# Optimization experiments

Hardware: AMD Instinct MI355X
Metric: run time of the kernel (lower is better)

## Reference

```python
import jax, jax.numpy as jnp
import numpy as np

LEAK = 0.1
K = 16  # nsample

def leaky(x):
    return jnp.where(x > 0, x, LEAK * x)

def setup_inputs() -> dict:
    key = jax.random.key(0)
    ks = jax.random.split(key, 16)
    B, N, C, D = 2, 8192, 128, 128
    s = 0.05
    return {
        "xyz1": jax.random.normal(ks[0], (B, 3, N), jnp.float32),
        "xyz2": jax.random.normal(ks[1], (B, 3, N), jnp.float32),
        "points1": jax.random.normal(ks[2], (B, C, N), jnp.float32),
        "points2": jax.random.normal(ks[3], (B, C, N), jnp.float32),
        "W_t11": jax.random.normal(ks[4], (D, C), jnp.float32) * s,
        "b_t11": jax.random.normal(ks[5], (D,), jnp.float32) * s,
        "W_t22": jax.random.normal(ks[6], (D, C), jnp.float32) * s,
        "b_t22": jax.random.normal(ks[7], (D,), jnp.float32) * s,
        "W_pos": jax.random.normal(ks[8], (D, 3), jnp.float32) * s,
        "b_pos": jax.random.normal(ks[9], (D,), jnp.float32) * s,
        "W_mlp1": jax.random.normal(ks[10], (D, D), jnp.float32) * s,
        "b_mlp1": jax.random.normal(ks[11], (D,), jnp.float32) * s,
        "W_mlp2": jax.random.normal(ks[12], (D, D), jnp.float32) * s,
        "b_mlp2": jax.random.normal(ks[13], (D,), jnp.float32) * s,
    }

def reference(xyz1, xyz2, points1, points2,
              W_t11, b_t11, W_t22, b_t22, W_pos, b_pos,
              W_mlp1, b_mlp1, W_mlp2, b_mlp2):
    # xyz*: [B,3,N], points*: [B,C,N]
    x1 = jnp.transpose(xyz1, (0, 2, 1))  # [B,N1,3]
    x2 = jnp.transpose(xyz2, (0, 2, 1))  # [B,N2,3]
    # 1x1 conv1d (t11/t22) -> [B,N,D]
    p1 = jnp.einsum('dc,bcn->bnd', W_t11, points1) + b_t11
    p2 = jnp.einsum('dc,bcn->bnd', W_t22, points2) + b_t22
    # squared distances [B,N1,N2]
    dist = (jnp.sum(x1 ** 2, -1)[:, :, None]
            + jnp.sum(x2 ** 2, -1)[:, None, :]
            - 2.0 * jnp.einsum('bnc,bmc->bnm', x1, x2))
    _, idx = jax.lax.top_k(-dist, K)  # [B,N1,K] nearest neighbors
    gather = jax.vmap(lambda pts, ix: pts[ix])  # per-batch fancy index
    nbr_xyz = gather(x2, idx)   # [B,N1,K,3]
    g2 = gather(p2, idx)        # [B,N1,K,D]
    direction = nbr_xyz - x1[:, :, None, :]
    pos = jnp.einsum('dc,bnkc->bnkd', W_pos, direction) + b_pos
    new_pts = leaky(g2 + p1[:, :, None, :] + pos)  # BN is Identity (use_bn=False)
    new_pts = leaky(jnp.einsum('dc,bnkc->bnkd', W_mlp1, new_pts) + b_mlp1)
    new_pts = leaky(jnp.einsum('dc,bnkc->bnkd', W_mlp2, new_pts) + b_mlp2)
    out = jnp.max(new_pts, axis=2)  # max over nsample -> [B,N1,D]
    return jnp.transpose(out, (0, 2, 1))  # [B,D,N1] like torch
```

## Files before the change

### kernel.cpp

```cpp
#include <hip/hip_runtime.h>
#include <hip/hip_bf16.h>

static constexpr int B_ = 2;
static constexpr int N_ = 8192;
static constexpr int C_ = 128;
static constexpr int D_ = 128;
static constexpr int K_ = 16;

typedef float f32x4 __attribute__((ext_vector_type(4)));
typedef short s16x8 __attribute__((ext_vector_type(8)));

__device__ __forceinline__ float lrelu(float x) { return fmaxf(x, 0.1f * x); }
__device__ __forceinline__ unsigned short f2bf(float f) {
  __hip_bfloat16 h = __float2bfloat16(f);
  unsigned short u;
  __builtin_memcpy(&u, &h, 2);
  return u;
}
__device__ __forceinline__ float bfl(unsigned int u) { return __uint_as_float(u << 16); }
__device__ __forceinline__ float bfh(unsigned int u) { return __uint_as_float(u & 0xffff0000u); }
__device__ __forceinline__ float rfl(float v) {
  return __uint_as_float((unsigned int)__builtin_amdgcn_readfirstlane((int)__float_as_uint(v)));
}

__global__ __launch_bounds__(256) void prep_kernel(
    const float* __restrict__ Wt11, const float* __restrict__ Wt22,
    const float* __restrict__ Wm1, const float* __restrict__ Wm2,
    const float* __restrict__ Wpos, const float* __restrict__ xyz2,
    const float* __restrict__ bt11, const float* __restrict__ bpos,
    float* __restrict__ Wt1T, float* __restrict__ Wt2T,
    unsigned short* __restrict__ w1bf, unsigned short* __restrict__ w2bf,
    float* __restrict__ wpx, float* __restrict__ wpy, float* __restrict__ wpz,
    float* __restrict__ b1c, f32x4* __restrict__ cand4) {
  int i = blockIdx.x * 256 + threadIdx.x;
  if (i < C_ * D_) {
    int d = i >> 7, c = i & 127;
    Wt1T[c * D_ + d] = Wt11[i];
    Wt2T[c * D_ + d] = Wt22[i];
    w1bf[i] = f2bf(Wm1[i]);
    w2bf[i] = f2bf(Wm2[i]);
    if (i < D_) {
      wpx[i] = Wpos[i * 3 + 0];
      wpy[i] = Wpos[i * 3 + 1];
      wpz[i] = Wpos[i * 3 + 2];
      b1c[i] = bt11[i] + bpos[i];
    }
    int bb = i >> 13, m = i & 8191;
    const float* s2 = xyz2 + (size_t)bb * 3 * N_;
    float x = s2[m], y = s2[N_ + m], z = s2[2 * N_ + m];
    f32x4 c4;
    c4[0] = -x; c4[1] = -y; c4[2] = -z;
    c4[3] = 0.5f * (x * x + y * y + z * z);
    cand4[(size_t)bb * N_ + m] = c4;
  }
}

__device__ __forceinline__ void conv_body(
    char* smem, int cbid,
    const float* __restrict__ pts, const float* __restrict__ WT,
    const float* __restrict__ bias, unsigned short* __restrict__ dst) {
  float (*tile)[64] = (float(*)[64])smem;
  int b = cbid >> 7;
  int n0 = (cbid & 127) << 6;
  int t = threadIdx.x;
  const float* src = pts + (size_t)b * C_ * N_ + n0;
  for (int i = t; i < C_ * 64; i += 256) {
    int c = i >> 6, nl = i & 63;
    tile[c][nl] = src[(size_t)c * N_ + nl];
  }
  __syncthreads();
  int w = t >> 6, lane = t & 63;
  int d0 = w * 32;
  float acc[32];
#pragma unroll
  for (int j = 0; j < 32; ++j) acc[j] = 0.f;
  for (int c = 0; c < C_; ++c) {
    float x = tile[c][lane];
    const f32x4* wp = (const f32x4*)(WT + c * D_ + d0);
#pragma unroll
    for (int j = 0; j < 8; ++j) {
      f32x4 wv = wp[j];
#pragma unroll
      for (int q = 0; q < 4; ++q) acc[4 * j + q] += wv[q] * x;
    }
  }
  unsigned short* drow = dst + ((size_t)(b * N_ + n0 + lane)) * D_ + d0;
#pragma unroll
  for (int j8 = 0; j8 < 4; ++j8) {
    uint4 ov;
    unsigned int us[8];
#pragma unroll
    for (int e = 0; e < 8; ++e)
      us[e] = f2bf(acc[8 * j8 + e] + bias[d0 + 8 * j8 + e]);
    ov.x = us[0] | (us[1] << 16);
    ov.y = us[2] | (us[3] << 16);
    ov.z = us[4] | (us[5] << 16);
    ov.w = us[6] | (us[7] << 16);
    *(uint4*)(drow + 8 * j8) = ov;
  }
}

__device__ __forceinline__ void knn_body(
    char* smem, int kbid,
    const float* __restrict__ xyz1, const f32x4* __restrict__ cand4,
    int* __restrict__ idx_out) {
  unsigned int (*idxbuf)[4][128] = (unsigned int(*)[4][128])smem;
  unsigned long long (*keybuf)[128] = (unsigned long long(*)[128])(smem + 8192);

  int b = kbid >> 9;
  int q0 = (kbid & 511) << 4;
  int t = threadIdx.x;
  int w = t >> 6, lane = t & 63;
  int qbase = q0 + (w << 2);

  const float* s1 = xyz1 + (size_t)b * 3 * N_;
  const f32x4* cb = cand4 + (size_t)b * N_;

  float qx[4], qy[4], qz[4], dmin[4];
#pragma unroll
  for (int qq = 0; qq < 4; ++qq) {
    int q = qbase + qq;
    qx[qq] = rfl(s1[q]);
    qy[qq] = rfl(s1[N_ + q]);
    qz[qq] = rfl(s1[2 * N_ + q]);
    dmin[qq] = 1e30f;
  }

#pragma unroll 4
  for (int i = 0; i < 128; ++i) {
    f32x4 c = cb[(i << 6) + lane];
#pragma unroll
    for (int qq = 0; qq < 4; ++qq) {
      float s = __builtin_fmaf(c[0], qx[qq],
                __builtin_fmaf(c[1], qy[qq],
                __builtin_fmaf(c[2], qz[qq], c[3])));
      dmin[qq] = fminf(dmin[qq], s);
    }
  }

  float thr[4];
#pragma unroll 1
  for (int qq = 0; qq < 4; ++qq) {
    unsigned int ukey = __float_as_uint(dmin[qq]);
    ukey ^= ((unsigned int)(((int)ukey) >> 31)) | 0x80000000u;
    unsigned int sel = 0;
    for (int bit = 31; bit >= 0; --bit) {
      unsigned int trial = sel | (1u << bit);
      int c_lt = __popcll(__ballot(ukey < trial));
      sel = (c_lt < 16) ? trial : sel;
    }
    unsigned int su = sel ^ ((sel & 0x80000000u) ? 0x80000000u : 0xFFFFFFFFu);
    float tf = __uint_as_float(su);
    thr[qq] = tf + (1e-4f + 4e-7f * fabsf(tf));
  }

  int cnt[4] = {0, 0, 0, 0};
  unsigned long long lmask = (1ull << lane) - 1ull;
#pragma unroll 2
  for (int i = 0; i < 128; ++i) {
    f32x4 c = cb[(i << 6) + lane];
    unsigned long long mk[4];
#pragma unroll
    for (int qq = 0; qq < 4; ++qq) {
      float s = __builtin_fmaf(c[0], qx[qq],
                __builtin_fmaf(c[1], qy[qq],
                __builtin_fmaf(c[2], qz[qq], c[3])));
      mk[qq] = __ballot(s <= thr[qq]);
    }
    unsigned long long united = mk[0] | mk[1] | mk[2] | mk[3];
    if (united) {
      int m = (i << 6) + lane;
#pragma unroll
      for (int qq = 0; qq < 4; ++qq) {
        if (mk[qq]) {
          if ((mk[qq] >> lane) & 1ull) {
            int pos = cnt[qq] + __popcll(mk[qq] & lmask);
            if (pos < 128) idxbuf[w][qq][pos] = (unsigned int)m;
          }
          cnt[qq] += __popcll(mk[qq]);
        }
      }
    }
  }

#pragma unroll 1
  for (int qq = 0; qq < 4; ++qq) {
    int Cq = cnt[qq] < 128 ? cnt[qq] : 128;
    bool v0 = lane < Cq;
    unsigned int i0v = v0 ? idxbuf[w][qq][lane] : 0u;
    f32x4 c0 = cb[i0v];
    float t0x = c0[0] + qx[qq], t0y = c0[1] + qy[qq], t0z = c0[2] + qz[qq];
    float d0 = __builtin_fmaf(t0x, t0x, __builtin_fmaf(t0y, t0y, t0z * t0z));
    unsigned long long key0 =
        v0 ? ((((unsigned long long)__float_as_uint(d0)) << 13) | i0v) : ~0ull;
    unsigned long long key1 = ~0ull;
    unsigned int i1v = 0;
    if (Cq > 64) {
      bool v1 = (lane + 64) < Cq;
      i1v = v1 ? idxbuf[w][qq][lane + 64] : 0u;
      f32x4 c1 = cb[i1v];
      float t1x = c1[0] + qx[qq], t1y = c1[1] + qy[qq], t1z = c1[2] + qz[qq];
      float d1 = __builtin_fmaf(t1x, t1x, __builtin_fmaf(t1y, t1y, t1z * t1z));
      key1 = v1 ? ((((unsigned long long)__float_as_uint(d1)) << 13) | i1v) : ~0ull;
    }
    keybuf[w][lane] = key0;
    keybuf[w][lane + 64] = key1;
    int rank0 = 0, rank1 = 0;
    for (int j = 0; j < Cq; ++j) {
      unsigned long long kj = keybuf[w][j];
      rank0 += (kj < key0) ? 1 : 0;
      rank1 += (kj < key1) ? 1 : 0;
    }
    int* dst = idx_out + (((size_t)b * N_ + (qbase + qq)) << 4);
    if (v0 && rank0 < K_) dst[rank0] = (int)i0v;
    if (key1 != ~0ull && rank1 < K_) dst[rank1] = (int)i1v;
  }
}

__global__ __launch_bounds__(256, 4) void fat_kernel(
    const float* __restrict__ xyz1, const f32x4* __restrict__ cand4,
    int* __restrict__ idx_out,
    const float* __restrict__ points1, const float* __restrict__ points2,
    const float* __restrict__ Wt1T, const float* __restrict__ Wt2T,
    const float* __restrict__ b1c, const float* __restrict__ bt22,
    unsigned short* __restrict__ p1b, unsigned short* __restrict__ p2b) {
  __shared__ __align__(16) char smem[32768];
  int bid = blockIdx.x;
  if (bid < 1024) {
    knn_body(smem, bid, xyz1, cand4, idx_out);
  } else if (bid < 1280) {
    conv_body(smem, bid - 1024, points1, Wt1T, b1c, p1b);
  } else {
    conv_body(smem, bid - 1280, points2, Wt2T, bt22, p2b);
  }
}

__global__ __launch_bounds__(256, 4) void fuse_kernel(
    const float* __restrict__ xyz1, const float* __restrict__ xyz2,
    const unsigned short* __restrict__ p1b, const unsigned short* __restrict__ p2b,
    const int* __restrict__ idxb,
    const unsigned short* __restrict__ w1bf, const unsigned short* __restrict__ w2bf,
    const float* __restrict__ wpx, const float* __restrict__ wpy,
    const float* __restrict__ wpz,
    const float* __restrict__ b1, const float* __restrict__ b2,
    float* __restrict__ out) {
  __shared__ unsigned char Abuf[32768];
  __shared__ float epib[4][8][32];

  int bid = blockIdx.x;
  int b = bid >> 10;
  int n0 = (bid & 1023) << 3;
  int t = threadIdx.x;
  int wv = t >> 6, lane = t & 63;
  int lrow = lane & 15, lk = lane >> 4;

  s16x8 wfr[2][4];
#pragma unroll
  for (int j2 = 0; j2 < 2; ++j2)
#pragma unroll
    for (int ks = 0; ks < 4; ++ks) {
      int row = wv * 32 + j2 * 16 + lrow;
      wfr[j2][ks] = *(const s16x8*)(w1bf + row * D_ + ks * 32 + lk * 8);
    }

  {
    int row = t >> 1, half = t & 1;
    int nl = row >> 4, kn = row & 15;
    int n = n0 + nl;
    int j = idxb[(((size_t)b * N_ + n) << 4) + kn];
    const float* s1 = xyz1 + (size_t)b * 3 * N_;
    const float* s2 = xyz2 + (size_t)b * 3 * N_;
    float dx = s2[j] - s1[n];
    float dy = s2[N_ + j] - s1[N_ + n];
    float dz = s2[2 * N_ + j] - s1[2 * N_ + n];
    const uint4* g2r = (const uint4*)(p2b + ((size_t)(b * N_ + j)) * D_ + half * 64);
    const uint4* p1r = (const uint4*)(p1b + ((size_t)(b * N_ + n)) * D_ + half * 64);
    int rswz = (row & 7) << 4;
#pragma unroll
    for (int it = 0; it < 8; ++it) {
      int dbase = half * 64 + it * 8;
      uint4 gv = g2r[it];
      uint4 pv = p1r[it];
      float g[8] = {bfl(gv.x), bfh(gv.x), bfl(gv.y), bfh(gv.y),
                    bfl(gv.z), bfh(gv.z), bfl(gv.w), bfh(gv.w)};
      float pp[8] = {bfl(pv.x), bfh(pv.x), bfl(pv.y), bfh(pv.y),
                     bfl(pv.z), bfh(pv.z), bfl(pv.w), bfh(pv.w)};
      f32x4 wxa = *(const f32x4*)(wpx + dbase);
      f32x4 wxb = *(const f32x4*)(wpx + dbase + 4);
      f32x4 wya = *(const f32x4*)(wpy + dbase);
      f32x4 wyb = *(const f32x4*)(wpy + dbase + 4);
      f32x4 wza = *(const f32x4*)(wpz + dbase);
      f32x4 wzb = *(const f32x4*)(wpz + dbase + 4);
      unsigned int us[8];
#pragma unroll
      for (int q = 0; q < 8; ++q) {
        float wx = q < 4 ? wxa[q] : wxb[q - 4];
        float wy = q < 4 ? wya[q] : wyb[q - 4];
        float wz = q < 4 ? wza[q] : wzb[q - 4];
        float v = __builtin_fmaf(wx, dx, __builtin_fmaf(wy, dy,
                  __builtin_fmaf(wz, dz, g[q] + pp[q])));
        us[q] = f2bf(lrelu(v));
      }
      uint4 val4;
      val4.x = us[0] | (us[1] << 16);
      val4.y = us[2] | (us[3] << 16);
      val4.z = us[4] | (us[5] << 16);
      val4.w = us[6] | (us[7] << 16);
      int off = (row << 8) + (dbase << 1);
      *(uint4*)(Abuf + (off ^ rswz)) = val4;
    }
  }
  __syncthreads();

  const f32x4 fzero = {0.f, 0.f, 0.f, 0.f};
  f32x4 acc[8][2];
#pragma unroll
  for (int m = 0; m < 8; ++m) { acc[m][0] = fzero; acc[m][1] = fzero; }

#pragma unroll
  for (int ks = 0; ks < 4; ++ks) {
#pragma unroll
    for (int m = 0; m < 8; ++m) {
      int rw = m * 16 + lrow;
      int off = (rw << 8) + (ks << 6) + (lk << 4);
      s16x8 afr = *(const s16x8*)(Abuf + (off ^ ((rw & 7) << 4)));
      acc[m][0] = __builtin_amdgcn_mfma_f32_16x16x32_bf16(afr, wfr[0][ks], acc[m][0], 0, 0, 0);
      acc[m][1] = __builtin_amdgcn_mfma_f32_16x16x32_bf16(afr, wfr[1][ks], acc[m][1], 0, 0, 0);
    }
  }
  __syncthreads();

#pragma unroll
  for (int j2 = 0; j2 < 2; ++j2)
#pragma unroll
    for (int ks = 0; ks < 4; ++ks) {
      int row = wv * 32 + j2 * 16 + lrow;
      wfr[j2][ks] = *(const s16x8*)(w2bf + row * D_ + ks * 32 + lk * 8);
    }

  {
    float bias1[2];
    bias1[0] = b1[wv * 32 + lrow];
    bias1[1] = b1[wv * 32 + 16 + lrow];
#pragma unroll
    for (int m = 0; m < 8; ++m)
#pragma unroll
      for (int j2 = 0; j2 < 2; ++j2)
#pragma unroll
        for (int r = 0; r < 4; ++r) {
          int rw = m * 16 + lk * 4 + r;
          int col = wv * 32 + j2 * 16 + lrow;
          unsigned short hv = f2bf(lrelu(acc[m][j2][r] + bias1[j2]));
          int off = (rw << 8) + (col << 1);
          *(unsigned short*)(Abuf + (off ^ ((rw & 7) << 4))) = hv;
        }
  }
  __syncthreads();

#pragma unroll
  for (int m = 0; m < 8; ++m) { acc[m][0] = fzero; acc[m][1] = fzero; }

#pragma unroll
  for (int ks = 0; ks < 4; ++ks) {
#pragma unroll
    for (int m = 0; m < 8; ++m) {
      int rw = m * 16 + lrow;
      int off = (rw << 8) + (ks << 6) + (lk << 4);
      s16x8 afr = *(const s16x8*)(Abuf + (off ^ ((rw & 7) << 4)));
      acc[m][0] = __builtin_amdgcn_mfma_f32_16x16x32_bf16(afr, wfr[0][ks], acc[m][0], 0, 0, 0);
      acc[m][1] = __builtin_amdgcn_mfma_f32_16x16x32_bf16(afr, wfr[1][ks], acc[m][1], 0, 0, 0);
    }
  }

  float bias2[2];
  bias2[0] = b2[wv * 32 + lrow];
  bias2[1] = b2[wv * 32 + 16 + lrow];
#pragma unroll
  for (int m = 0; m < 8; ++m) {
#pragma unroll
    for (int j2 = 0; j2 < 2; ++j2) {
      float mx = -1e30f;
#pragma unroll
      for (int r = 0; r < 4; ++r) mx = fmaxf(mx, lrelu(acc[m][j2][r] + bias2[j2]));
      mx = fmaxf(mx, __shfl_xor(mx, 16, 64));
      mx = fmaxf(mx, __shfl_xor(mx, 32, 64));
      if (lk == 0) epib[wv][m][j2 * 16 + lrow] = mx;
    }
  }
  {
    int dl = lane >> 1, nh = lane & 1;
    f32x4 o;
#pragma unroll
    for (int i2 = 0; i2 < 4; ++i2) o[i2] = epib[wv][nh * 4 + i2][dl];
    *(f32x4*)(out + ((size_t)(b * D_ + wv * 32 + dl)) * N_ + n0 + nh * 4) = o;
  }
}

extern "C" void kernel_launch(void* const* d_in, const int* in_sizes, int n_in,
                              void* d_out, int out_size, void* d_ws, size_t ws_size,
                              hipStream_t stream) {
  (void)in_sizes; (void)n_in; (void)out_size; (void)ws_size;
  const float* xyz1    = (const float*)d_in[0];
  const float* xyz2    = (const float*)d_in[1];
  const float* points1 = (const float*)d_in[2];
  const float* points2 = (const float*)d_in[3];
  const float* W_t11   = (const float*)d_in[4];
  const float* b_t11   = (const float*)d_in[5];
  const float* W_t22   = (const float*)d_in[6];
  const float* b_t22   = (const float*)d_in[7];
  const float* W_pos   = (const float*)d_in[8];
  const float* b_pos   = (const float*)d_in[9];
  const float* W_mlp1  = (const float*)d_in[10];
  const float* b_mlp1  = (const float*)d_in[11];
  const float* W_mlp2  = (const float*)d_in[12];
  const float* b_mlp2  = (const float*)d_in[13];
  float* out = (float*)d_out;

  char* ws = (char*)d_ws;
  unsigned short* p1b  = (unsigned short*)(ws);
  unsigned short* p2b  = (unsigned short*)(ws + 4194304);
  float* Wt1T          = (float*)(ws + 8388608);
  float* Wt2T          = (float*)(ws + 8454144);
  unsigned short* w1bf = (unsigned short*)(ws + 8519680);
  unsigned short* w2bf = (unsigned short*)(ws + 8552448);
  float* wpx           = (float*)(ws + 8585216);
  float* wpy           = (float*)(ws + 8585728);
  float* wpz           = (float*)(ws + 8586240);
  f32x4* cand4         = (f32x4*)(ws + 8586752);
  int* idxws           = (int*)(ws + 8848896);
  float* b1c           = (float*)(ws + 9897472);

  prep_kernel<<<64, 256, 0, stream>>>(W_t11, W_t22, W_mlp1, W_mlp2, W_pos, xyz2,
                                      b_t11, b_pos,
                                      Wt1T, Wt2T, w1bf, w2bf, wpx, wpy, wpz,
                                      b1c, cand4);
  fat_kernel<<<1536, 256, 0, stream>>>(xyz1, cand4, idxws,
                                       points1, points2, Wt1T, Wt2T,
                                       b1c, b_t22, p1b, p2b);
  fuse_kernel<<<B_ * 1024, 256, 0, stream>>>(xyz1, xyz2, p1b, p2b, idxws,
                                             w1bf, w2bf, wpx, wpy, wpz,
                                             b_mlp1, b_mlp2, out);
}
```

Baseline: 181.4 us.

## Stage KNN candidate chunks in shared memory and raise occupancy bound

The KNN scan loops now cooperatively copy 1024-candidate chunks into LDS and let each wavefront read its candidates from shared memory instead of global/L2. The ballot compaction loop drops the union-mask branch and processes each query unconditionally. The launch bounds min-blocks hint is raised from 4 to 5. The cost is extra __syncthreads per chunk and possible register pressure from the higher occupancy hint.

```diff
diff --git a/kernel.cpp b/kernel.cpp
--- a/kernel.cpp
+++ b/kernel.cpp
@@ -104,8 +104,9 @@
     char* smem, int kbid,
     const float* __restrict__ xyz1, const f32x4* __restrict__ cand4,
     int* __restrict__ idx_out) {
-  unsigned int (*idxbuf)[4][128] = (unsigned int(*)[4][128])smem;
-  unsigned long long (*keybuf)[128] = (unsigned long long(*)[128])(smem + 8192);
+  f32x4* cbuf = (f32x4*)smem;
+  unsigned int (*idxbuf)[4][128] = (unsigned int(*)[4][128])(smem + 16384);
+  unsigned long long (*keybuf)[128] = (unsigned long long(*)[128])(smem + 24576);
 
   int b = kbid >> 9;
   int q0 = (kbid & 511) << 4;
@@ -126,15 +127,24 @@
     dmin[qq] = 1e30f;
   }
 
+  for (int ch = 0; ch < 8; ++ch) {
+    __syncthreads();
+    {
+      const f32x4* src = cb + (ch << 10);
+#pragma unroll
+      for (int i = 0; i < 4; ++i) cbuf[t + (i << 8)] = src[t + (i << 8)];
+    }
+    __syncthreads();
 #pragma unroll 4
-  for (int i = 0; i < 128; ++i) {
-    f32x4 c = cb[(i << 6) + lane];
-#pragma unroll
-    for (int qq = 0; qq < 4; ++qq) {
-      float s = __builtin_fmaf(c[0], qx[qq],
-                __builtin_fmaf(c[1], qy[qq],
-                __builtin_fmaf(c[2], qz[qq], c[3])));
-      dmin[qq] = fminf(dmin[qq], s);
+    for (int i = 0; i < 16; ++i) {
+      f32x4 c = cbuf[(i << 6) + lane];
+#pragma unroll
+      for (int qq = 0; qq < 4; ++qq) {
+        float s = __builtin_fmaf(c[0], qx[qq],
+                  __builtin_fmaf(c[1], qy[qq],
+                  __builtin_fmaf(c[2], qz[qq], c[3])));
+        dmin[qq] = fminf(dmin[qq], s);
+      }
     }
   }
 
@@ -156,29 +166,29 @@
 
   int cnt[4] = {0, 0, 0, 0};
   unsigned long long lmask = (1ull << lane) - 1ull;
+  for (int ch = 0; ch < 8; ++ch) {
+    __syncthreads();
+    {
+      const f32x4* src = cb + (ch << 10);
+#pragma unroll
+      for (int i = 0; i < 4; ++i) cbuf[t + (i << 8)] = src[t + (i << 8)];
+    }
+    __syncthreads();
 #pragma unroll 2
-  for (int i = 0; i < 128; ++i) {
-    f32x4 c = cb[(i << 6) + lane];
-    unsigned long long mk[4];
-#pragma unroll
-    for (int qq = 0; qq < 4; ++qq) {
-      float s = __builtin_fmaf(c[0], qx[qq],
-                __builtin_fmaf(c[1], qy[qq],
-                __builtin_fmaf(c[2], qz[qq], c[3])));
-      mk[qq] = __ballot(s <= thr[qq]);
-    }
-    unsigned long long united = mk[0] | mk[1] | mk[2] | mk[3];
-    if (united) {
-      int m = (i << 6) + lane;
+    for (int i = 0; i < 16; ++i) {
+      f32x4 c = cbuf[(i << 6) + lane];
+      int m = (ch << 10) + (i << 6) + lane;
 #pragma unroll
       for (int qq = 0; qq < 4; ++qq) {
-        if (mk[qq]) {
-          if ((mk[qq] >> lane) & 1ull) {
-            int pos = cnt[qq] + __popcll(mk[qq] & lmask);
-            if (pos < 128) idxbuf[w][qq][pos] = (unsigned int)m;
-          }
-          cnt[qq] += __popcll(mk[qq]);
+        float s = __builtin_fmaf(c[0], qx[qq],
+                  __builtin_fmaf(c[1], qy[qq],
+                  __builtin_fmaf(c[2], qz[qq], c[3])));
+        unsigned long long mk = __ballot(s <= thr[qq]);
+        if ((mk >> lane) & 1ull) {
+          int pos = cnt[qq] + __popcll(mk & lmask);
+          if (pos < 128) idxbuf[w][qq][pos] = (unsigned int)m;
         }
+        cnt[qq] += __popcll(mk);
       }
     }
   }
@@ -217,7 +227,7 @@
   }
 }
 
-__global__ __launch_bounds__(256, 4) void fat_kernel(
+__global__ __launch_bounds__(256, 5) void fat_kernel(
     const float* __restrict__ xyz1, const f32x4* __restrict__ cand4,
     int* __restrict__ idx_out,
     const float* __restrict__ points1, const float* __restrict__ points2,
```

After: 191.3 us. 1.05x slower.

## Process eight queries per wave in KNN with prefetch and LDS atomic compaction

Applied to the files above, without the earlier changes.

Each wave now handles eight query points instead of four, so every candidate load is reused across twice as many distance computations, and the KNN grid is halved to match. Candidate loads are software-prefetched four iterations ahead in both scan passes. The ballot/popcount compaction of threshold hits is replaced by per-lane LDS atomicAdd on per-query counters, and occupancy in launch bounds is raised from 4 to 5. The risks are higher register pressure from eight query states plus prefetch registers under the tighter bound, nondeterministic ordering of the collected candidate indices (final ranking still uses index tie-breaks), and fewer KNN blocks to fill the GPU.

```diff
diff --git a/kernel.cpp b/kernel.cpp
--- a/kernel.cpp
+++ b/kernel.cpp
@@ -104,21 +104,24 @@
     char* smem, int kbid,
     const float* __restrict__ xyz1, const f32x4* __restrict__ cand4,
     int* __restrict__ idx_out) {
-  unsigned int (*idxbuf)[4][128] = (unsigned int(*)[4][128])smem;
-  unsigned long long (*keybuf)[128] = (unsigned long long(*)[128])(smem + 8192);
-
-  int b = kbid >> 9;
-  int q0 = (kbid & 511) << 4;
+  unsigned int (*idxbuf)[8][128] = (unsigned int(*)[8][128])smem;
+  unsigned long long (*keybuf)[128] = (unsigned long long(*)[128])(smem + 16384);
+  unsigned int (*icnt)[8] = (unsigned int(*)[8])(smem + 20480);
+
+  int b = kbid >> 8;
+  int q0 = (kbid & 255) << 5;
   int t = threadIdx.x;
   int w = t >> 6, lane = t & 63;
-  int qbase = q0 + (w << 2);
+  int qbase = q0 + (w << 3);
 
   const float* s1 = xyz1 + (size_t)b * 3 * N_;
   const f32x4* cb = cand4 + (size_t)b * N_;
 
-  float qx[4], qy[4], qz[4], dmin[4];
-#pragma unroll
-  for (int qq = 0; qq < 4; ++qq) {
+  if (lane < 8) icnt[w][lane] = 0u;
+
+  float qx[8], qy[8], qz[8], dmin[8];
+#pragma unroll
+  for (int qq = 0; qq < 8; ++qq) {
     int q = qbase + qq;
     qx[qq] = rfl(s1[q]);
     qy[qq] = rfl(s1[N_ + q]);
@@ -126,21 +129,29 @@
     dmin[qq] = 1e30f;
   }
 
-#pragma unroll 4
-  for (int i = 0; i < 128; ++i) {
-    f32x4 c = cb[(i << 6) + lane];
-#pragma unroll
-    for (int qq = 0; qq < 4; ++qq) {
-      float s = __builtin_fmaf(c[0], qx[qq],
-                __builtin_fmaf(c[1], qy[qq],
-                __builtin_fmaf(c[2], qz[qq], c[3])));
-      dmin[qq] = fminf(dmin[qq], s);
-    }
-  }
-
-  float thr[4];
+  {
+    f32x4 p0 = cb[lane], p1 = cb[64 + lane], p2 = cb[128 + lane], p3 = cb[192 + lane];
+    auto proc1 = [&](f32x4 c) {
+#pragma unroll
+      for (int qq = 0; qq < 8; ++qq) {
+        float s = __builtin_fmaf(c[0], qx[qq],
+                  __builtin_fmaf(c[1], qy[qq],
+                  __builtin_fmaf(c[2], qz[qq], c[3])));
+        dmin[qq] = fminf(dmin[qq], s);
+      }
+    };
+    for (int i = 0; i < 124; i += 4) {
+      f32x4 c0 = p0; p0 = cb[((i + 4) << 6) + lane]; proc1(c0);
+      f32x4 c1 = p1; p1 = cb[((i + 5) << 6) + lane]; proc1(c1);
+      f32x4 c2 = p2; p2 = cb[((i + 6) << 6) + lane]; proc1(c2);
+      f32x4 c3 = p3; p3 = cb[((i + 7) << 6) + lane]; proc1(c3);
+    }
+    proc1(p0); proc1(p1); proc1(p2); proc1(p3);
+  }
+
+  float thr[8];
 #pragma unroll 1
-  for (int qq = 0; qq < 4; ++qq) {
+  for (int qq = 0; qq < 8; ++qq) {
     unsigned int ukey = __float_as_uint(dmin[qq]);
     ukey ^= ((unsigned int)(((int)ukey) >> 31)) | 0x80000000u;
     unsigned int sel = 0;
@@ -154,38 +165,36 @@
     thr[qq] = tf + (1e-4f + 4e-7f * fabsf(tf));
   }
 
-  int cnt[4] = {0, 0, 0, 0};
-  unsigned long long lmask = (1ull << lane) - 1ull;
-#pragma unroll 2
-  for (int i = 0; i < 128; ++i) {
-    f32x4 c = cb[(i << 6) + lane];
-    unsigned long long mk[4];
-#pragma unroll
-    for (int qq = 0; qq < 4; ++qq) {
-      float s = __builtin_fmaf(c[0], qx[qq],
-                __builtin_fmaf(c[1], qy[qq],
-                __builtin_fmaf(c[2], qz[qq], c[3])));
-      mk[qq] = __ballot(s <= thr[qq]);
-    }
-    unsigned long long united = mk[0] | mk[1] | mk[2] | mk[3];
-    if (united) {
-      int m = (i << 6) + lane;
-#pragma unroll
-      for (int qq = 0; qq < 4; ++qq) {
-        if (mk[qq]) {
-          if ((mk[qq] >> lane) & 1ull) {
-            int pos = cnt[qq] + __popcll(mk[qq] & lmask);
-            if (pos < 128) idxbuf[w][qq][pos] = (unsigned int)m;
-          }
-          cnt[qq] += __popcll(mk[qq]);
+  {
+    f32x4 p0 = cb[lane], p1 = cb[64 + lane], p2 = cb[128 + lane], p3 = cb[192 + lane];
+    auto proc2 = [&](f32x4 c, int m) {
+#pragma unroll
+      for (int qq = 0; qq < 8; ++qq) {
+        float s = __builtin_fmaf(c[0], qx[qq],
+                  __builtin_fmaf(c[1], qy[qq],
+                  __builtin_fmaf(c[2], qz[qq], c[3])));
+        if (s <= thr[qq]) {
+          unsigned int pos = atomicAdd(&icnt[w][qq], 1u);
+          if (pos < 128u) idxbuf[w][qq][pos] = (unsigned int)m;
         }
       }
-    }
+    };
+    for (int i = 0; i < 124; i += 4) {
+      f32x4 c0 = p0; p0 = cb[((i + 4) << 6) + lane]; proc2(c0, (i << 6) + lane);
+      f32x4 c1 = p1; p1 = cb[((i + 5) << 6) + lane]; proc2(c1, ((i + 1) << 6) + lane);
+      f32x4 c2 = p2; p2 = cb[((i + 6) << 6) + lane]; proc2(c2, ((i + 2) << 6) + lane);
+      f32x4 c3 = p3; p3 = cb[((i + 7) << 6) + lane]; proc2(c3, ((i + 3) << 6) + lane);
+    }
+    proc2(p0, (124 << 6) + lane);
+    proc2(p1, (125 << 6) + lane);
+    proc2(p2, (126 << 6) + lane);
+    proc2(p3, (127 << 6) + lane);
   }
 
 #pragma unroll 1
-  for (int qq = 0; qq < 4; ++qq) {
-    int Cq = cnt[qq] < 128 ? cnt[qq] : 128;
+  for (int qq = 0; qq < 8; ++qq) {
+    int Cq = (int)icnt[w][qq];
+    if (Cq > 128) Cq = 128;
     bool v0 = lane < Cq;
     unsigned int i0v = v0 ? idxbuf[w][qq][lane] : 0u;
     f32x4 c0 = cb[i0v];
@@ -217,7 +226,7 @@
   }
 }
 
-__global__ __launch_bounds__(256, 4) void fat_kernel(
+__global__ __launch_bounds__(256, 5) void fat_kernel(
     const float* __restrict__ xyz1, const f32x4* __restrict__ cand4,
     int* __restrict__ idx_out,
     const float* __restrict__ points1, const float* __restrict__ points2,
@@ -226,12 +235,12 @@
     unsigned short* __restrict__ p1b, unsigned short* __restrict__ p2b) {
   __shared__ __align__(16) char smem[32768];
   int bid = blockIdx.x;
-  if (bid < 1024) {
+  if (bid < 512) {
     knn_body(smem, bid, xyz1, cand4, idx_out);
-  } else if (bid < 1280) {
-    conv_body(smem, bid - 1024, points1, Wt1T, b1c, p1b);
+  } else if (bid < 768) {
+    conv_body(smem, bid - 512, points1, Wt1T, b1c, p1b);
   } else {
-    conv_body(smem, bid - 1280, points2, Wt2T, bt22, p2b);
+    conv_body(smem, bid - 768, points2, Wt2T, bt22, p2b);
   }
 }
 
@@ -434,7 +443,7 @@
                                       b_t11, b_pos,
                                       Wt1T, Wt2T, w1bf, w2bf, wpx, wpy, wpz,
                                       b1c, cand4);
-  fat_kernel<<<1536, 256, 0, stream>>>(xyz1, cand4, idxws,
+  fat_kernel<<<1024, 256, 0, stream>>>(xyz1, cand4, idxws,
                                        points1, points2, Wt1T, Wt2T,
                                        b1c, b_t22, p1b, p2b);
   fuse_kernel<<<B_ * 1024, 256, 0, stream>>>(xyz1, xyz2, p1b, p2b, idxws,
```

Measured after the change: 159.4 us. 1.14x faster.
